# Kernel tuning notes

Measured on AMD Instinct MI355X. Metric: run time of the kernel, lower is better.

Reference implementation:

```python
import jax, jax.numpy as jnp
import numpy as np

B, C_IN, C_OUT, N = 8, 256, 256, 2048
SCALE = 10.0
EPSILON = 1e-3
LEAKY_SLOPE = 0.01
NORM_EPS = 1e-12


def setup_inputs() -> dict:
    key = jax.random.key(0)
    k1, k2, k3, k4 = jax.random.split(key, 4)
    query = jax.random.normal(k1, (B, C_IN, N), dtype=jnp.float32)
    key_t = jax.random.normal(k2, (B, C_IN, N), dtype=jnp.float32)
    # Shared key/query conv (self_attention=True), 1x1 Conv1d weights (no bias)
    fan1 = 1.0 / np.sqrt(C_IN)
    fan2 = 1.0 / np.sqrt(2 * C_IN)
    W1 = jax.random.uniform(k3, (2 * C_IN, C_IN), jnp.float32, -fan1, fan1)
    W2 = jax.random.uniform(k4, (C_OUT, 2 * C_IN), jnp.float32, -fan2, fan2)
    return {"query": query, "key": key_t, "W1": W1, "W2": W2}


def _nonlinearity(x, W1, W2):
    # 1x1 Conv1d == channel-mixing matmul; x: [B, C, N]
    h = jnp.einsum("oc,bcn->bon", W1, x)
    h = jnp.where(h >= 0, h, LEAKY_SLOPE * h)
    return jnp.einsum("oc,bcn->bon", W2, h)


def _l2norm(x):
    # F.normalize(x, dim=1): divide by max(||x||_2, eps)
    n = jnp.sqrt(jnp.sum(x * x, axis=1, keepdims=True))
    return x / jnp.maximum(n, NORM_EPS)


def reference(query, key, W1, W2):
    q_out = _l2norm(_nonlinearity(query, W1, W2))  # [B, C_out, Nq]
    k_out = _l2norm(_nonlinearity(key, W1, W2))    # [B, C_out, Nk]
    scores = jnp.einsum("bcq,bck->bqk", q_out, k_out) * SCALE  # [B, Nq, Nk]
    weights = jax.nn.softmax(scores, axis=-1)
    weights = jnp.where(weights > EPSILON, weights, 0.0)  # nn.Threshold(eps, 0)
    return (weights, key)
```

## Files before the change

### kernel.cpp

```cpp
#include <hip/hip_runtime.h>
#include <hip/hip_bf16.h>
#include <math.h>

#define B_      8
#define CIN     256
#define CMID    512
#define COUT    256
#define N_      2048
#define SCALE_  10.0f
#define EPS_THR 1e-3f
#define NORM_EPS_ 1e-12f

typedef __attribute__((ext_vector_type(8))) short short8;
typedef __attribute__((ext_vector_type(4))) float f32x4;

__device__ __forceinline__ ushort f2bf(float x) {
    union { float f; uint u; } v; v.f = x;
    uint r = v.u + 0x7FFF + ((v.u >> 16) & 1);
    return (ushort)(r >> 16);
}
__device__ __forceinline__ float bf2f(ushort h) {
    union { uint u; float f; } v; v.u = ((uint)h) << 16;
    return v.f;
}
__device__ __forceinline__ void gload_lds16(const void* g, void* l) {
    __builtin_amdgcn_global_load_lds((const __attribute__((address_space(1))) void*)g,
                                     (__attribute__((address_space(3))) void*)l, 16, 0, 0);
}

__global__ __launch_bounds__(256) void prep_w(const float* __restrict__ W1,
                                              const float* __restrict__ W2,
                                              ushort* __restrict__ W1b,
                                              ushort* __restrict__ W2b) {
    int idx = blockIdx.x * 256 + threadIdx.x;
    W1b[idx] = f2bf(W1[idx]);
    W2b[idx] = f2bf(W2[idx]);
}

#define ASTRIDE 40
__global__ __launch_bounds__(512) void conv1_fused(const float* __restrict__ q,
                                                   const float* __restrict__ k,
                                                   const ushort* __restrict__ W1b,
                                                   ushort* __restrict__ H) {
    __shared__ ushort As[64 * ASTRIDE];
    __shared__ ushort Bs[512 * 32];
    int tid = threadIdx.x;
    int lane = tid & 63, wave = tid >> 6;
    int g = lane >> 4, cl = lane & 15;
    int bx = blockIdx.x;
    int half = bx >> 8;
    int u = bx & 255;
    int pb = u & 7, pj = u >> 3;
    size_t m0 = ((size_t)half * 256 + (size_t)pb * 32 + pj) * 64;
    const float* xsrc = (m0 < 16384) ? q : k;
    int b = (int)((m0 >> 11) & 7);
    int nbase = (int)(m0 & 2047);
    const float* xp = xsrc + ((size_t)b * CIN + wave * 4) * N_ + nbase + lane;

    f32x4 acc[4][4];
#pragma unroll
    for (int i = 0; i < 4; ++i)
#pragma unroll
        for (int j = 0; j < 4; ++j) acc[i][j] = (f32x4)0.f;

    for (int k0 = 0; k0 < CIN; k0 += 32) {
#pragma unroll
        for (int si = 0; si < 4; ++si) {
            int s = tid + si * 512;
            gload_lds16(W1b + (size_t)(s >> 2) * CIN + k0 + (s & 3) * 8, Bs + s * 8);
        }
        float v0 = xp[(size_t)(k0 + 0) * N_];
        float v1 = xp[(size_t)(k0 + 1) * N_];
        float v2 = xp[(size_t)(k0 + 2) * N_];
        float v3 = xp[(size_t)(k0 + 3) * N_];
        ushort4 wv;
        wv.x = f2bf(v0); wv.y = f2bf(v1); wv.z = f2bf(v2); wv.w = f2bf(v3);
        *(ushort4*)&As[lane * ASTRIDE + wave * 4] = wv;
        __syncthreads();

        short8 af[4], bfr[4];
#pragma unroll
        for (int mi = 0; mi < 4; ++mi)
            af[mi] = *(const short8*)&As[(mi * 16 + cl) * ASTRIDE + g * 8];
#pragma unroll
        for (int ni = 0; ni < 4; ++ni)
            bfr[ni] = *(const short8*)&Bs[(wave * 64 + ni * 16 + cl) * 32 + g * 8];
#pragma unroll
        for (int mi = 0; mi < 4; ++mi)
#pragma unroll
            for (int ni = 0; ni < 4; ++ni)
                acc[mi][ni] = __builtin_amdgcn_mfma_f32_16x16x32_bf16(af[mi], bfr[ni], acc[mi][ni], 0, 0, 0);
        __syncthreads();
    }

#pragma unroll
    for (int mi = 0; mi < 4; ++mi)
#pragma unroll
        for (int ni = 0; ni < 4; ++ni)
#pragma unroll
            for (int r = 0; r < 4; ++r) {
                float v = acc[mi][ni][r];
                v = (v >= 0.f) ? v : 0.01f * v;
                H[(m0 + mi * 16 + g * 4 + r) * CMID + wave * 64 + ni * 16 + cl] = f2bf(v);
            }
}

__global__ __launch_bounds__(512) void conv2_norm(const ushort* __restrict__ H,
                                                  const ushort* __restrict__ W2b,
                                                  ushort* __restrict__ QK) {
    __shared__ ushort As[128 * 32];
    __shared__ ushort Bs[256 * 32];
    __shared__ float red[4][128];
    int tid = threadIdx.x;
    int lane = tid & 63, wave = tid >> 6;
    int wm = wave >> 2, wn = wave & 3;
    int g = lane >> 4, cl = lane & 15;
    int bx = blockIdx.x;
    int half = bx >> 7;
    int u = bx & 127;
    int pb = u & 7, pj = u >> 3;
    size_t m0 = ((size_t)half * 128 + (size_t)pb * 16 + pj) * 128;

    f32x4 acc[4][4];
#pragma unroll
    for (int i = 0; i < 4; ++i)
#pragma unroll
        for (int j = 0; j < 4; ++j) acc[i][j] = (f32x4)0.f;

    for (int k0 = 0; k0 < CMID; k0 += 32) {
        gload_lds16(H + (m0 + (tid >> 2)) * CMID + k0 + (tid & 3) * 8, As + tid * 8);
#pragma unroll
        for (int si = 0; si < 2; ++si) {
            int s = tid + si * 512;
            gload_lds16(W2b + (size_t)(s >> 2) * CMID + k0 + (s & 3) * 8, Bs + s * 8);
        }
        __syncthreads();
        short8 af[4], bfr[4];
#pragma unroll
        for (int mi = 0; mi < 4; ++mi)
            af[mi] = *(const short8*)&As[(wm * 64 + mi * 16 + cl) * 32 + g * 8];
#pragma unroll
        for (int ni = 0; ni < 4; ++ni)
            bfr[ni] = *(const short8*)&Bs[(wn * 64 + ni * 16 + cl) * 32 + g * 8];
#pragma unroll
        for (int mi = 0; mi < 4; ++mi)
#pragma unroll
            for (int ni = 0; ni < 4; ++ni)
                acc[mi][ni] = __builtin_amdgcn_mfma_f32_16x16x32_bf16(af[mi], bfr[ni], acc[mi][ni], 0, 0, 0);
        __syncthreads();
    }

#pragma unroll
    for (int mi = 0; mi < 4; ++mi)
#pragma unroll
        for (int r = 0; r < 4; ++r) {
            float s = 0.f;
#pragma unroll
            for (int ni = 0; ni < 4; ++ni) { float v = acc[mi][ni][r]; s += v * v; }
#pragma unroll
            for (int off = 1; off < 16; off <<= 1) s += __shfl_xor(s, off, 64);
            if (cl == 0) red[wn][wm * 64 + mi * 16 + g * 4 + r] = s;
        }
    __syncthreads();
#pragma unroll
    for (int mi = 0; mi < 4; ++mi)
#pragma unroll
        for (int r = 0; r < 4; ++r) {
            int row = wm * 64 + mi * 16 + g * 4 + r;
            size_t row_g = m0 + row;
            float tot = red[0][row] + red[1][row] + red[2][row] + red[3][row];
            float inv = 1.0f / fmaxf(sqrtf(tot), NORM_EPS_);
            size_t pbase = (row_g >> 4) * 4096 + (size_t)(row_g & 15) * 8;
#pragma unroll
            for (int ni = 0; ni < 4; ++ni) {
                int kcol = wn * 64 + ni * 16 + cl;
                size_t off = pbase + (size_t)(kcol >> 5) * 512
                           + (size_t)((kcol >> 3) & 3) * 128 + (kcol & 7);
                QK[off] = f2bf(acc[mi][ni][r] * inv);
            }
        }
}

#define ESTRIDE 2052
__global__ __launch_bounds__(512, 2) void scores_softmax(const ushort* __restrict__ QK,
                                                         float* __restrict__ out) {
    __shared__ ushort eLDS[32 * ESTRIDE];
    __shared__ float red[8][32];
    int bid = blockIdx.x;
    int b = bid & 7;
    int m0 = (bid >> 3) * 32;
    int tid = threadIdx.x;
    int lane = tid & 63, wave = tid >> 6;
    int g = lane >> 4, cl = lane & 15;

    const ushort* Qf = QK + ((size_t)(b * N_ + m0) >> 4) * 4096;
    const ushort* Kf = QK + ((size_t)(16384 + b * N_ + wave * 256) >> 4) * 4096;

    short8 af0[8], af1[8];
#pragma unroll
    for (int ks = 0; ks < 8; ++ks) {
        af0[ks] = *(const short8*)(Qf + ks * 512 + lane * 8);
        af1[ks] = *(const short8*)(Qf + 4096 + ks * 512 + lane * 8);
    }

    float rs0[4] = {0.f, 0.f, 0.f, 0.f}, rs1[4] = {0.f, 0.f, 0.f, 0.f};
    int ecol = wave * 256 + cl;

#pragma unroll
    for (int ct = 0; ct < 16; ++ct) {
        f32x4 a0 = (f32x4)0.f, a1 = (f32x4)0.f;
#pragma unroll
        for (int ks = 0; ks < 8; ++ks) {
            short8 bfr = *(const short8*)(Kf + (size_t)ct * 4096 + ks * 512 + lane * 8);
            a0 = __builtin_amdgcn_mfma_f32_16x16x32_bf16(af0[ks], bfr, a0, 0, 0, 0);
            a1 = __builtin_amdgcn_mfma_f32_16x16x32_bf16(af1[ks], bfr, a1, 0, 0, 0);
        }
#pragma unroll
        for (int r = 0; r < 4; ++r) {
            float e0 = __expf((a0[r] - 1.0f) * SCALE_);
            rs0[r] += e0;
            eLDS[(g * 4 + r) * ESTRIDE + ecol + ct * 16] = f2bf(e0);
            float e1 = __expf((a1[r] - 1.0f) * SCALE_);
            rs1[r] += e1;
            eLDS[(16 + g * 4 + r) * ESTRIDE + ecol + ct * 16] = f2bf(e1);
        }
    }

#pragma unroll
    for (int r = 0; r < 4; ++r) {
        float s = rs0[r];
#pragma unroll
        for (int off = 1; off < 16; off <<= 1) s += __shfl_xor(s, off, 64);
        if (cl == 0) red[wave][g * 4 + r] = s;
        float s1 = rs1[r];
#pragma unroll
        for (int off = 1; off < 16; off <<= 1) s1 += __shfl_xor(s1, off, 64);
        if (cl == 0) red[wave][16 + g * 4 + r] = s1;
    }
    __syncthreads();

    float inv_[4];
#pragma unroll
    for (int rr = 0; rr < 4; ++rr) {
        int row = wave * 4 + rr;
        float t = 0.f;
#pragma unroll
        for (int w = 0; w < 8; ++w) t += red[w][row];
        inv_[rr] = 1.0f / t;
    }

    float* ob = out + (size_t)b * N_ * N_ + (size_t)m0 * N_;
#pragma unroll
    for (int rr = 0; rr < 4; ++rr) {
        int row = wave * 4 + rr;
        const ushort* ep = &eLDS[row * ESTRIDE];
        float* orow = ob + (size_t)row * N_;
#pragma unroll
        for (int j = 0; j < 8; ++j) {
            int c = j * 256 + lane * 4;
            ushort4 ev = *(const ushort4*)&ep[c];
            f32x4 w;
            float t;
            t = bf2f(ev.x) * inv_[rr]; w.x = (t > EPS_THR) ? t : 0.f;
            t = bf2f(ev.y) * inv_[rr]; w.y = (t > EPS_THR) ? t : 0.f;
            t = bf2f(ev.z) * inv_[rr]; w.z = (t > EPS_THR) ? t : 0.f;
            t = bf2f(ev.w) * inv_[rr]; w.w = (t > EPS_THR) ? t : 0.f;
            __builtin_nontemporal_store(w, (f32x4*)&orow[c]);
        }
    }
}

__global__ __launch_bounds__(256) void copy_key(const float* __restrict__ in,
                                                float* __restrict__ dst, int n4) {
    int i = blockIdx.x * 256 + threadIdx.x;
    if (i < n4) {
        f32x4 v = ((const f32x4*)in)[i];
        __builtin_nontemporal_store(v, &((f32x4*)dst)[i]);
    }
}

extern "C" void kernel_launch(void* const* d_in, const int* in_sizes, int n_in,
                              void* d_out, int out_size, void* d_ws, size_t ws_size,
                              hipStream_t stream) {
    const float* q  = (const float*)d_in[0];
    const float* k  = (const float*)d_in[1];
    const float* W1 = (const float*)d_in[2];
    const float* W2 = (const float*)d_in[3];
    float* out = (float*)d_out;

    ushort* W1b = (ushort*)d_ws;
    ushort* W2b = W1b + 131072;
    ushort* QK  = W2b + 131072;

    ushort* H = (ushort*)d_out;

    prep_w<<<512, 256, 0, stream>>>(W1, W2, W1b, W2b);
    conv1_fused<<<512, 512, 0, stream>>>(q, k, W1b, H);
    conv2_norm<<<256, 512, 0, stream>>>(H, W2b, QK);
    scores_softmax<<<512, 512, 0, stream>>>(QK, out);
    copy_key<<<4096, 256, 0, stream>>>(k, out + (size_t)B_ * N_ * N_, (B_ * CIN * N_) / 4);
}
```

Before: 107.1 us.

## Recompute QK scores in second pass instead of staging exponentials in LDS

The scores_softmax kernel no longer stores bf16 exponentials in a large LDS buffer. It runs the MFMA score computation twice: once to accumulate row sums and again to produce normalized, thresholded weights that are written straight to global memory. This frees about 128KB of LDS per block, which could raise occupancy, at the cost of doubling the matmul and exp work. The output stores become scalar 4-byte writes with 16-lane column groups instead of 16-byte vector stores, which may hurt write coalescing.

Measured after the change: 131.9 us. +23.2%, slower.

```diff
diff --git a/kernel.cpp b/kernel.cpp
--- a/kernel.cpp
+++ b/kernel.cpp
@@ -18,10 +18,6 @@
     union { float f; uint u; } v; v.f = x;
     uint r = v.u + 0x7FFF + ((v.u >> 16) & 1);
     return (ushort)(r >> 16);
-}
-__device__ __forceinline__ float bf2f(ushort h) {
-    union { uint u; float f; } v; v.u = ((uint)h) << 16;
-    return v.f;
 }
 __device__ __forceinline__ void gload_lds16(const void* g, void* l) {
     __builtin_amdgcn_global_load_lds((const __attribute__((address_space(1))) void*)g,
@@ -181,10 +177,8 @@
         }
 }
 
-#define ESTRIDE 2052
 __global__ __launch_bounds__(512, 2) void scores_softmax(const ushort* __restrict__ QK,
                                                          float* __restrict__ out) {
-    __shared__ ushort eLDS[32 * ESTRIDE];
     __shared__ float red[8][32];
     int bid = blockIdx.x;
     int b = bid & 7;
@@ -204,25 +198,22 @@
     }
 
     float rs0[4] = {0.f, 0.f, 0.f, 0.f}, rs1[4] = {0.f, 0.f, 0.f, 0.f};
-    int ecol = wave * 256 + cl;
-
-#pragma unroll
+
     for (int ct = 0; ct < 16; ++ct) {
+        short8 bfr[8];
+#pragma unroll
+        for (int ks = 0; ks < 8; ++ks)
+            bfr[ks] = *(const short8*)(Kf + (size_t)ct * 4096 + ks * 512 + lane * 8);
         f32x4 a0 = (f32x4)0.f, a1 = (f32x4)0.f;
 #pragma unroll
         for (int ks = 0; ks < 8; ++ks) {
-            short8 bfr = *(const short8*)(Kf + (size_t)ct * 4096 + ks * 512 + lane * 8);
-            a0 = __builtin_amdgcn_mfma_f32_16x16x32_bf16(af0[ks], bfr, a0, 0, 0, 0);
-            a1 = __builtin_amdgcn_mfma_f32_16x16x32_bf16(af1[ks], bfr, a1, 0, 0, 0);
-        }
-#pragma unroll
-        for (int r = 0; r < 4; ++r) {
-            float e0 = __expf((a0[r] - 1.0f) * SCALE_);
-            rs0[r] += e0;
-            eLDS[(g * 4 + r) * ESTRIDE + ecol + ct * 16] = f2bf(e0);
-            float e1 = __expf((a1[r] - 1.0f) * SCALE_);
-            rs1[r] += e1;
-            eLDS[(16 + g * 4 + r) * ESTRIDE + ecol + ct * 16] = f2bf(e1);
+            a0 = __builtin_amdgcn_mfma_f32_16x16x32_bf16(af0[ks], bfr[ks], a0, 0, 0, 0);
+            a1 = __builtin_amdgcn_mfma_f32_16x16x32_bf16(af1[ks], bfr[ks], a1, 0, 0, 0);
+        }
+#pragma unroll
+        for (int r = 0; r < 4; ++r) {
+            rs0[r] += __expf((a0[r] - 1.0f) * SCALE_);
+            rs1[r] += __expf((a1[r] - 1.0f) * SCALE_);
         }
     }
 
@@ -239,33 +230,37 @@
     }
     __syncthreads();
 
-    float inv_[4];
-#pragma unroll
-    for (int rr = 0; rr < 4; ++rr) {
-        int row = wave * 4 + rr;
-        float t = 0.f;
-#pragma unroll
-        for (int w = 0; w < 8; ++w) t += red[w][row];
-        inv_[rr] = 1.0f / t;
-    }
-
-    float* ob = out + (size_t)b * N_ * N_ + (size_t)m0 * N_;
-#pragma unroll
-    for (int rr = 0; rr < 4; ++rr) {
-        int row = wave * 4 + rr;
-        const ushort* ep = &eLDS[row * ESTRIDE];
-        float* orow = ob + (size_t)row * N_;
-#pragma unroll
-        for (int j = 0; j < 8; ++j) {
-            int c = j * 256 + lane * 4;
-            ushort4 ev = *(const ushort4*)&ep[c];
-            f32x4 w;
-            float t;
-            t = bf2f(ev.x) * inv_[rr]; w.x = (t > EPS_THR) ? t : 0.f;
-            t = bf2f(ev.y) * inv_[rr]; w.y = (t > EPS_THR) ? t : 0.f;
-            t = bf2f(ev.z) * inv_[rr]; w.z = (t > EPS_THR) ? t : 0.f;
-            t = bf2f(ev.w) * inv_[rr]; w.w = (t > EPS_THR) ? t : 0.f;
-            __builtin_nontemporal_store(w, (f32x4*)&orow[c]);
+    float inv0[4], inv1[4];
+#pragma unroll
+    for (int r = 0; r < 4; ++r) {
+        int row = g * 4 + r;
+        float t0 = 0.f, t1 = 0.f;
+#pragma unroll
+        for (int w = 0; w < 8; ++w) { t0 += red[w][row]; t1 += red[w][16 + row]; }
+        inv0[r] = 1.0f / t0;
+        inv1[r] = 1.0f / t1;
+    }
+
+    float* ob = out + (size_t)b * N_ * N_ + (size_t)m0 * N_ + wave * 256;
+    for (int ct = 0; ct < 16; ++ct) {
+        short8 bfr[8];
+#pragma unroll
+        for (int ks = 0; ks < 8; ++ks)
+            bfr[ks] = *(const short8*)(Kf + (size_t)ct * 4096 + ks * 512 + lane * 8);
+        f32x4 a0 = (f32x4)0.f, a1 = (f32x4)0.f;
+#pragma unroll
+        for (int ks = 0; ks < 8; ++ks) {
+            a0 = __builtin_amdgcn_mfma_f32_16x16x32_bf16(af0[ks], bfr[ks], a0, 0, 0, 0);
+            a1 = __builtin_amdgcn_mfma_f32_16x16x32_bf16(af1[ks], bfr[ks], a1, 0, 0, 0);
+        }
+#pragma unroll
+        for (int r = 0; r < 4; ++r) {
+            float w0 = __expf((a0[r] - 1.0f) * SCALE_) * inv0[r];
+            w0 = (w0 > EPS_THR) ? w0 : 0.f;
+            __builtin_nontemporal_store(w0, &ob[(size_t)(g * 4 + r) * N_ + ct * 16 + cl]);
+            float w1 = __expf((a1[r] - 1.0f) * SCALE_) * inv1[r];
+            w1 = (w1 > EPS_THR) ? w1 : 0.f;
+            __builtin_nontemporal_store(w1, &ob[(size_t)(16 + g * 4 + r) * N_ + ct * 16 + cl]);
         }
     }
 }
```
